# Optimization experiments

Hardware: AMD Instinct MI355X
Metric: run time of the kernel (lower is better)

The kernel has to match this reference:

```python
import jax, jax.numpy as jnp
import numpy as np
import math

B, N, D, H, FF, L = 256, 200, 128, 8, 512, 2
KD = D // H  # key/val dim per head
NEG_INF = -1e30  # used via -jnp.inf where safe


def setup_inputs() -> dict:
    key = jax.random.key(0)
    ks = jax.random.split(key, 32)
    s = 0.08
    inp = {
        "coords": jax.random.uniform(ks[0], (B, N, 2), jnp.float32),
        "demand": jax.random.uniform(ks[1], (B, N), jnp.float32) * 0.01,
        # init embeddings
        "w_depot": jax.random.normal(ks[2], (2, D), jnp.float32) * s,
        "b_depot": jax.random.normal(ks[3], (D,), jnp.float32) * s,
        "w_init": jax.random.normal(ks[4], (3, D), jnp.float32) * s,
        "b_init": jax.random.normal(ks[5], (D,), jnp.float32) * s,
        # encoder layers (stacked over L)
        "Wq": jax.random.normal(ks[6], (L, H, D, KD), jnp.float32) * s,
        "Wk": jax.random.normal(ks[7], (L, H, D, KD), jnp.float32) * s,
        "Wv": jax.random.normal(ks[8], (L, H, D, KD), jnp.float32) * s,
        "Wo": jax.random.normal(ks[9], (L, H, KD, D), jnp.float32) * s,
        "ff1_w": jax.random.normal(ks[10], (L, D, FF), jnp.float32) * s,
        "ff1_b": jax.random.normal(ks[11], (L, FF), jnp.float32) * s,
        "ff2_w": jax.random.normal(ks[12], (L, FF, D), jnp.float32) * s,
        "ff2_b": jax.random.normal(ks[13], (L, D), jnp.float32) * s,
        "n1_g": jnp.ones((L, D), jnp.float32),
        "n1_b": jnp.zeros((L, D), jnp.float32),
        "n2_g": jnp.ones((L, D), jnp.float32),
        "n2_b": jnp.zeros((L, D), jnp.float32),
        # decoder projections
        "w_proj_nodes": jax.random.normal(ks[14], (D, 3 * D), jnp.float32) * s,
        "w_fixed": jax.random.normal(ks[15], (D, D), jnp.float32) * s,
        "w_step": jax.random.normal(ks[16], (D + 1, D), jnp.float32) * s,
        "w_out": jax.random.normal(ks[17], (D, D), jnp.float32) * s,
    }
    return inp


def _batch_norm(x, g, b):
    # torch BatchNorm1d on flattened (B*N, D), training-mode batch stats
    m = x.mean(axis=(0, 1))
    v = x.var(axis=(0, 1))
    return g * (x - m) * jax.lax.rsqrt(v + 1e-5) + b


def _mha(x, Wq, Wk, Wv, Wo):
    # x: [B,N,D]; W*: [H,D,KD]; Wo: [H,KD,D]
    Q = jnp.einsum('bni,hik->hbnk', x, Wq)
    K = jnp.einsum('bni,hik->hbnk', x, Wk)
    V = jnp.einsum('bni,hik->hbnk', x, Wv)
    scale = 1.0 / math.sqrt(KD)
    attn = jax.nn.softmax(scale * jnp.einsum('hbnk,hbmk->hbnm', Q, K), axis=-1)
    heads = jnp.einsum('hbnm,hbmk->hbnk', attn, V)
    return jnp.einsum('hbnk,hkd->bnd', heads, Wo)


def _forward(coords, demand, w_depot, b_depot, w_init, b_init,
             Wq, Wk, Wv, Wo, ff1_w, ff1_b, ff2_w, ff2_b,
             n1_g, n1_b, n2_g, n2_b, w_proj_nodes, w_fixed, w_step, w_out):
    # ---- _init_embed ----
    depot_emb = coords[:, :1, :2] @ w_depot + b_depot                      # [B,1,D]
    node_feat = jnp.concatenate([coords[:, 1:, :], demand[:, 1:, None]], -1)
    node_emb = node_feat @ w_init + b_init                                 # [B,N-1,D]
    h = jnp.concatenate([depot_emb, node_emb], axis=1)                     # [B,N,D]

    # ---- GraphAttentionEncoder ----
    for l in range(L):
        h = _batch_norm(h + _mha(h, Wq[l], Wk[l], Wv[l], Wo[l]), n1_g[l], n1_b[l])
        ff = jnp.maximum(h @ ff1_w[l] + ff1_b[l], 0.0) @ ff2_w[l] + ff2_b[l]
        h = _batch_norm(h + ff, n2_g[l], n2_b[l])

    # ---- _precompute ----
    fixed_ctx = h.mean(axis=1) @ w_fixed                                   # [B,D]
    proj = h @ w_proj_nodes                                                # [B,N,3D]
    gk, gv, lk = jnp.split(proj, 3, axis=-1)
    gk = gk.reshape(B, N, H, KD).transpose(2, 0, 1, 3)                     # [H,B,N,KD]
    gv = gv.reshape(B, N, H, KD).transpose(2, 0, 1, 3)                     # [H,B,N,KD]

    inv_sqrt_kd = 1.0 / math.sqrt(KD)
    inv_sqrt_d = 1.0 / math.sqrt(D)
    barange = jnp.arange(B)

    def step(carry, _):
        visited, cur, used = carry
        cur_emb = h[barange, cur]                                          # [B,D]
        ctx = jnp.concatenate([cur_emb, (1.0 - used)[:, None]], -1)        # [B,D+1]
        q = fixed_ctx + ctx @ w_step                                       # [B,D]
        qh = q.reshape(B, H, KD).transpose(1, 0, 2)                        # [H,B,KD]
        compat = jnp.einsum('hbk,hbnk->hbn', qh, gk) * inv_sqrt_kd         # [H,B,N]
        compat = jnp.where(visited[None], -jnp.inf, compat)                # mask_inner
        attn = jax.nn.softmax(compat, axis=-1)
        gl = jnp.einsum('hbn,hbnk->hbk', attn, gv)                         # [H,B,KD]
        final_q = gl.transpose(1, 0, 2).reshape(B, D) @ w_out              # [B,D]
        logits = jnp.einsum('bd,bnd->bn', final_q, lk) * inv_sqrt_d
        logits = jnp.tanh(logits) * 10.0                                   # tanh_clipping
        logits = jnp.where(visited, -jnp.inf, logits)                      # mask_logits
        logp = jax.nn.log_softmax(logits, axis=-1)                         # temp = 1.0
        sel = jnp.argmax(logp, axis=-1)                                    # greedy decode
        visited = visited.at[barange, sel].set(True)
        used = used + demand[barange, sel]
        return (visited, sel, used), (logp, sel)

    visited0 = jnp.zeros((B, N), bool).at[:, 0].set(True)  # start at depot
    cur0 = jnp.zeros((B,), jnp.int32)
    used0 = jnp.zeros((B,), jnp.float32)
    _, (logps, sels) = jax.lax.scan(step, (visited0, cur0, used0), None, length=N - 1)
    log_p = logps.transpose(1, 0, 2)   # [B, N-1, N]
    pi = sels.transpose(1, 0)          # [B, N-1]
    return log_p, pi


def reference(coords, demand, w_depot, b_depot, w_init, b_init,
              Wq, Wk, Wv, Wo, ff1_w, ff1_b, ff2_w, ff2_b,
              n1_g, n1_b, n2_g, n2_b, w_proj_nodes, w_fixed, w_step, w_out):
    return _forward(coords, demand, w_depot, b_depot, w_init, b_init,
                    Wq, Wk, Wv, Wo, ff1_w, ff1_b, ff2_w, ff2_b,
                    n1_g, n1_b, n2_g, n2_b, w_proj_nodes, w_fixed, w_step, w_out)
```

## Files before the change

kernel.cpp:

```cpp
#include <hip/hip_runtime.h>
#include <math.h>

#define NB 256
#define NN 200
#define ND 128
#define NH 8
#define NFF 512
#define MROWS (NB*NN)

#define NEG_BIG (-1.0e30f)

#define GBM 128
#define GBN 128
#define GBK 16
__global__ __launch_bounds__(256) void k_gemm(const float* __restrict__ A,
    const float* __restrict__ B, const float* __restrict__ bias,
    float* __restrict__ C, int M, int N, int K, int flags)
{
  __shared__ float As[GBK][GBM];
  __shared__ float Bs[GBK][GBN];
  const int t = threadIdx.x;
  const int tx = t & 15, ty = t >> 4;
  const int row0 = blockIdx.y * GBM, col0 = blockIdx.x * GBN;
  float acc[8][8] = {};
  for (int k0 = 0; k0 < K; k0 += GBK) {
    {
      int m = t >> 1, kb = (t & 1) * 8;
      const float* src = A + (size_t)(row0 + m) * K + k0 + kb;
      float4 v0 = *(const float4*)(src);
      float4 v1 = *(const float4*)(src + 4);
      As[kb+0][m] = v0.x; As[kb+1][m] = v0.y; As[kb+2][m] = v0.z; As[kb+3][m] = v0.w;
      As[kb+4][m] = v1.x; As[kb+5][m] = v1.y; As[kb+6][m] = v1.z; As[kb+7][m] = v1.w;
    }
    {
      int kk = t >> 4, nb = (t & 15) * 8;
      const float* src = B + (size_t)(k0 + kk) * N + col0 + nb;
      float4 v0 = *(const float4*)(src);
      float4 v1 = *(const float4*)(src + 4);
      *(float4*)&Bs[kk][nb]   = v0;
      *(float4*)&Bs[kk][nb+4] = v1;
    }
    __syncthreads();
    #pragma unroll
    for (int kk = 0; kk < GBK; ++kk) {
      float a[8], bv[8];
      *(float4*)&a[0]  = *(const float4*)&As[kk][ty*8];
      *(float4*)&a[4]  = *(const float4*)&As[kk][ty*8+4];
      *(float4*)&bv[0] = *(const float4*)&Bs[kk][tx*8];
      *(float4*)&bv[4] = *(const float4*)&Bs[kk][tx*8+4];
      #pragma unroll
      for (int i = 0; i < 8; ++i)
        #pragma unroll
        for (int j = 0; j < 8; ++j)
          acc[i][j] += a[i] * bv[j];
    }
    __syncthreads();
  }
  #pragma unroll
  for (int i = 0; i < 8; ++i) {
    int r = row0 + ty*8 + i;
    float* crow = C + (size_t)r * N + col0 + tx*8;
    #pragma unroll
    for (int j = 0; j < 8; ++j) {
      float v = acc[i][j];
      if (bias) v += bias[col0 + tx*8 + j];
      if (flags & 1) v += crow[j];
      if (flags & 2) v = fmaxf(v, 0.0f);
      crow[j] = v;
    }
  }
}

__global__ void k_pack_wqkv(const float* __restrict__ Wq, const float* __restrict__ Wk,
                            const float* __restrict__ Wv, float* __restrict__ outp)
{
  int idx = blockIdx.x * 256 + threadIdx.x;
  if (idx >= 2*128*384) return;
  int l = idx / (128*384); int r = idx % (128*384);
  int d = r / 384; int j = r % 384;
  int sel = j >> 7; int hk = j & 127; int h = hk >> 4; int k = hk & 15;
  const float* W = sel == 0 ? Wq : (sel == 1 ? Wk : Wv);
  outp[idx] = W[((size_t)(l*8 + h)*128 + d)*16 + k];
}

__global__ void k_init(const float* __restrict__ coords, const float* __restrict__ demand,
                       const float* __restrict__ w_depot, const float* __restrict__ b_depot,
                       const float* __restrict__ w_init, const float* __restrict__ b_init,
                       float* __restrict__ h)
{
  int idx = blockIdx.x * 256 + threadIdx.x;
  if (idx >= NB*NN*ND) return;
  int d = idx & 127; int bn = idx >> 7; int n = bn % NN; int b = bn / NN;
  float cx = coords[(size_t)(b*NN + n)*2], cy = coords[(size_t)(b*NN + n)*2 + 1];
  float v;
  if (n == 0) v = cx*w_depot[d] + cy*w_depot[128+d] + b_depot[d];
  else        v = cx*w_init[d] + cy*w_init[128+d] + demand[b*NN+n]*w_init[256+d] + b_init[d];
  h[idx] = v;
}

__global__ __launch_bounds__(256) void k_attn(const float* __restrict__ qkv, float* __restrict__ out)
{
  __shared__ float Qs[NN][16], Ks[NN][16], Vs[NN][16];
  __shared__ float Ss[32][NN];
  const int b = blockIdx.x >> 3, hd = blockIdx.x & 7;
  const int t = threadIdx.x;
  const float* base = qkv + (size_t)b * NN * 384 + hd * 16;
  for (int e = t; e < NN * 16; e += 256) {
    int n = e >> 4, k = e & 15;
    const float* p = base + (size_t)n * 384;
    Qs[n][k] = p[k];
    Ks[n][k] = p[128 + k];
    Vs[n][k] = p[256 + k];
  }
  __syncthreads();
  const int i = t >> 3;
  const int jl = t & 7;
  for (int i0 = 0; i0 < NN; i0 += 32) {
    int ii = i0 + i;
    if (ii < NN) {
      float4 q0 = *(const float4*)&Qs[ii][0];
      float4 q1 = *(const float4*)&Qs[ii][4];
      float4 q2 = *(const float4*)&Qs[ii][8];
      float4 q3 = *(const float4*)&Qs[ii][12];
      for (int j = jl; j < NN; j += 8) {
        const float* kr = &Ks[j][0];
        float s = q0.x*kr[0] + q0.y*kr[1] + q0.z*kr[2]  + q0.w*kr[3]
                + q1.x*kr[4] + q1.y*kr[5] + q1.z*kr[6]  + q1.w*kr[7]
                + q2.x*kr[8] + q2.y*kr[9] + q2.z*kr[10] + q2.w*kr[11]
                + q3.x*kr[12]+ q3.y*kr[13]+ q3.z*kr[14] + q3.w*kr[15];
        Ss[i][j] = s * 0.25f;
      }
      float m = -INFINITY;
      for (int j = jl; j < NN; j += 8) m = fmaxf(m, Ss[i][j]);
      m = fmaxf(m, __shfl_xor(m, 1));
      m = fmaxf(m, __shfl_xor(m, 2));
      m = fmaxf(m, __shfl_xor(m, 4));
      float sum = 0.f;
      for (int j = jl; j < NN; j += 8) { float p = expf(Ss[i][j] - m); Ss[i][j] = p; sum += p; }
      sum += __shfl_xor(sum, 1);
      sum += __shfl_xor(sum, 2);
      sum += __shfl_xor(sum, 4);
      float inv = 1.0f / sum;
      float a0 = 0.f, a1 = 0.f;
      int k0 = jl * 2;
      for (int j = 0; j < NN; ++j) {
        float p = Ss[i][j];
        a0 += p * Vs[j][k0];
        a1 += p * Vs[j][k0+1];
      }
      float* o = out + ((size_t)b * NN + ii) * ND + hd * 16 + k0;
      o[0] = a0 * inv; o[1] = a1 * inv;
    }
  }
}

__global__ __launch_bounds__(256) void k_bn_stats(const float* __restrict__ x, float* __restrict__ partial)
{
  int jb = blockIdx.x, t = threadIdx.x;
  int c = t & 127, half = t >> 7;
  const float* base = x + (size_t)jb * NN * ND;
  float s = 0.f, ss = 0.f;
  for (int r = half; r < NN; r += 2) {
    float v = base[(size_t)r * ND + c];
    s += v; ss += v * v;
  }
  __shared__ float s1[256], s2[256];
  s1[t] = s; s2[t] = ss;
  __syncthreads();
  if (t < 128) {
    partial[(size_t)jb*128 + t]         = s1[t] + s1[t+128];
    partial[32768 + (size_t)jb*128 + t] = s2[t] + s2[t+128];
  }
}

__global__ void k_bn_finish(const float* __restrict__ partial, const float* __restrict__ g,
                            const float* __restrict__ bb, float* __restrict__ scsh)
{
  int c = threadIdx.x;
  float s = 0.f, ss = 0.f;
  for (int jb = 0; jb < 256; ++jb) {
    s  += partial[jb*128 + c];
    ss += partial[32768 + jb*128 + c];
  }
  float mean = s * (1.0f/51200.0f);
  float var  = ss * (1.0f/51200.0f) - mean*mean;
  float sc = g[c] * rsqrtf(var + 1e-5f);
  scsh[c] = sc;
  scsh[128 + c] = bb[c] - mean * sc;
}

__global__ void k_bn_apply(float* __restrict__ x, const float* __restrict__ scsh)
{
  int idx = blockIdx.x * 256 + threadIdx.x;
  if (idx >= NB*NN*ND) return;
  int c = idx & 127;
  x[idx] = x[idx] * scsh[c] + scsh[128 + c];
}

__global__ __launch_bounds__(256) void k_mean(const float* __restrict__ h, float* __restrict__ meanh)
{
  int b = blockIdx.x, t = threadIdx.x;
  int d = t & 127, half = t >> 7;
  float s = 0.f;
  for (int n = half; n < NN; n += 2) s += h[((size_t)b*NN + n)*ND + d];
  __shared__ float sm[256];
  sm[t] = s;
  __syncthreads();
  if (t < 128) meanh[b*ND + t] = (sm[t] + sm[t+128]) * (1.0f/200.0f);
}

__global__ __launch_bounds__(1024) void k_decode(
    const float* __restrict__ proj, const float* __restrict__ hproj,
    const float* __restrict__ fixedc, const float* __restrict__ w_step,
    const float* __restrict__ w_out, const float* __restrict__ demand,
    float* __restrict__ out_logp, float* __restrict__ out_pi)
{
  const int b = blockIdx.x;
  const int t = threadIdx.x;
  __shared__ __align__(16) float q[ND];
  __shared__ __align__(16) float fq[ND];
  __shared__ float fc[ND], wlast[ND];
  __shared__ float cmat[NH][NN];
  __shared__ float logits[NN];
  __shared__ float glp[8][ND], gl[ND];
  __shared__ float fqp[8][ND];
  __shared__ int idxl[NN];
  __shared__ int upos[NN];
  __shared__ int visited[NN];
  __shared__ int curs;
  __shared__ float useds;
  __shared__ float redf[16];
  __shared__ int redi[16];
  __shared__ float selv_s, lse_s;
  __shared__ int seln_s;

  if (t < ND) { fc[t] = fixedc[b*ND + t]; wlast[t] = w_step[128*ND + t]; }
  if (t < NN) {
    visited[t] = (t == 0) ? 1 : 0;
    upos[t] = t - 1;
    if (t < NN - 1) idxl[t] = t + 1;
  }
  if (t == 0) { curs = 0; useds = 0.0f; }
  __syncthreads();

  const float* pb = proj + (size_t)b * NN * 384;
  const int g = t >> 4, j16 = t & 15;
  const int qi = j16 * 4;

  int U = NN - 1;
  for (int step = 0; step < NN - 1; ++step) {
    if (t < ND) q[t] = fc[t] + hproj[((size_t)b*NN + curs)*ND + t] + (1.0f - useds)*wlast[t];
    __syncthreads();

    for (int u = g; u < U; u += 64) {
      const float* row = pb + (size_t)idxl[u]*384;
      float4 r0 = *(const float4*)(row + qi);
      float4 r1 = *(const float4*)(row + 64 + qi);
      float4 qa = *(const float4*)(q + qi);
      float4 qb = *(const float4*)(q + 64 + qi);
      float p0 = r0.x*qa.x + r0.y*qa.y + r0.z*qa.z + r0.w*qa.w;
      float p1 = r1.x*qb.x + r1.y*qb.y + r1.z*qb.z + r1.w*qb.w;
      p0 += __shfl_xor(p0, 1); p0 += __shfl_xor(p0, 2);
      p1 += __shfl_xor(p1, 1); p1 += __shfl_xor(p1, 2);
      if ((j16 & 3) == 0) {
        cmat[j16 >> 2][u]       = p0 * 0.25f;
        cmat[4 + (j16 >> 2)][u] = p1 * 0.25f;
      }
    }
    __syncthreads();

    if (t < 256) {
      int h = t >> 5, l5 = t & 31;
      float m = -INFINITY;
      for (int u = l5; u < U; u += 32) m = fmaxf(m, cmat[h][u]);
      #pragma unroll
      for (int mm = 1; mm < 32; mm <<= 1) m = fmaxf(m, __shfl_xor(m, mm));
      float s = 0.f;
      for (int u = l5; u < U; u += 32) { float p = expf(cmat[h][u] - m); cmat[h][u] = p; s += p; }
      #pragma unroll
      for (int mm = 1; mm < 32; mm <<= 1) s += __shfl_xor(s, mm);
      float inv = 1.0f / s;
      for (int u = l5; u < U; u += 32) cmat[h][u] *= inv;
    }
    __syncthreads();

    {
      int c = t >> 7, i = t & 127;
      float acc = 0.f;
      int hh = i >> 4;
      for (int u = c; u < U; u += 8) acc += cmat[hh][u] * pb[(size_t)idxl[u]*384 + 128 + i];
      glp[c][i] = acc;
    }
    __syncthreads();
    if (t < ND)
      gl[t] = ((glp[0][t] + glp[1][t]) + (glp[2][t] + glp[3][t]))
            + ((glp[4][t] + glp[5][t]) + (glp[6][t] + glp[7][t]));
    __syncthreads();

    {
      int c = t >> 7, d = t & 127;
      float acc = 0.f;
      const float* wb = w_out + (size_t)(c*16)*ND + d;
      #pragma unroll
      for (int i = 0; i < 16; ++i) acc += gl[c*16 + i] * wb[(size_t)i*ND];
      fqp[c][d] = acc;
    }
    __syncthreads();
    if (t < ND)
      fq[t] = ((fqp[0][t] + fqp[1][t]) + (fqp[2][t] + fqp[3][t]))
            + ((fqp[4][t] + fqp[5][t]) + (fqp[6][t] + fqp[7][t]));
    __syncthreads();

    for (int u = g; u < U; u += 64) {
      const float* row = pb + (size_t)idxl[u]*384 + 256;
      float4 r0 = *(const float4*)(row + qi);
      float4 r1 = *(const float4*)(row + 64 + qi);
      float4 fa = *(const float4*)(fq + qi);
      float4 fb = *(const float4*)(fq + 64 + qi);
      float p = r0.x*fa.x + r0.y*fa.y + r0.z*fa.z + r0.w*fa.w
              + r1.x*fb.x + r1.y*fb.y + r1.z*fb.z + r1.w*fb.w;
      p += __shfl_xor(p, 1); p += __shfl_xor(p, 2);
      p += __shfl_xor(p, 4); p += __shfl_xor(p, 8);
      if (j16 == 0) logits[u] = tanhf(p * 0.088388347648318447f) * 10.0f;
    }
    __syncthreads();

    float mv = -INFINITY; int mn = 0x7fffffff;
    for (int u = t; u < U; u += 1024) {
      float v = logits[u]; int n = idxl[u];
      if (v > mv || (v == mv && n < mn)) { mv = v; mn = n; }
    }
    #pragma unroll
    for (int mm = 1; mm < 64; mm <<= 1) {
      float ov = __shfl_xor(mv, mm); int on = __shfl_xor(mn, mm);
      if (ov > mv || (ov == mv && on < mn)) { mv = ov; mn = on; }
    }
    if ((t & 63) == 0) { redf[t >> 6] = mv; redi[t >> 6] = mn; }
    __syncthreads();
    if (t == 0) {
      for (int w = 1; w < 16; ++w)
        if (redf[w] > mv || (redf[w] == mv && redi[w] < mn)) { mv = redf[w]; mn = redi[w]; }
      selv_s = mv; seln_s = mn;
    }
    __syncthreads();
    float gmax = selv_s;
    float se = 0.f;
    for (int u = t; u < U; u += 1024) se += expf(logits[u] - gmax);
    #pragma unroll
    for (int mm = 1; mm < 64; mm <<= 1) se += __shfl_xor(se, mm);
    if ((t & 63) == 0) redf[t >> 6] = se;
    __syncthreads();
    if (t == 0) {
      float s = 0.f;
      for (int w = 0; w < 16; ++w) s += redf[w];
      lse_s = gmax + logf(s);
    }
    __syncthreads();
    float lse = lse_s;

    float* orow = out_logp + ((size_t)b*(NN-1) + step)*NN;
    if (t < NN) {
      int u = upos[t];
      float lv = logits[u < 0 ? 0 : u] - lse;
      orow[t] = visited[t] ? NEG_BIG : lv;
    }
    __syncthreads();
    if (t == 0) {
      int sel = seln_s;
      out_pi[(size_t)b*(NN-1) + step] = (float)sel;
      int us = upos[sel];
      int last = idxl[U-1];
      idxl[us] = last;
      upos[last] = us;
      visited[sel] = 1;
      upos[sel] = -1;
      curs = sel;
      useds += demand[b*NN + sel];
    }
    __syncthreads();
    --U;
  }
}

extern "C" void kernel_launch(void* const* d_in, const int* in_sizes, int n_in,
                              void* d_out, int out_size, void* d_ws, size_t ws_size,
                              hipStream_t stream)
{
  (void)in_sizes; (void)n_in; (void)out_size; (void)ws_size;
  const float* coords  = (const float*)d_in[0];
  const float* demand  = (const float*)d_in[1];
  const float* w_depot = (const float*)d_in[2];
  const float* b_depot = (const float*)d_in[3];
  const float* w_init  = (const float*)d_in[4];
  const float* b_init  = (const float*)d_in[5];
  const float* Wq      = (const float*)d_in[6];
  const float* Wk      = (const float*)d_in[7];
  const float* Wv      = (const float*)d_in[8];
  const float* Wo      = (const float*)d_in[9];
  const float* ff1w    = (const float*)d_in[10];
  const float* ff1b    = (const float*)d_in[11];
  const float* ff2w    = (const float*)d_in[12];
  const float* ff2b    = (const float*)d_in[13];
  const float* n1g     = (const float*)d_in[14];
  const float* n1b     = (const float*)d_in[15];
  const float* n2g     = (const float*)d_in[16];
  const float* n2b     = (const float*)d_in[17];
  const float* wproj   = (const float*)d_in[18];
  const float* wfixed  = (const float*)d_in[19];
  const float* wstep   = (const float*)d_in[20];
  const float* wout    = (const float*)d_in[21];
  float* out = (float*)d_out;

  float* ws = (float*)d_ws;
  float* h       = ws;
  float* big     = h + 6553600;
  float* attnout = big + (size_t)MROWS * 384;
  float* hproj   = attnout;
  float* meanh   = big + 26214400;
  float* fixedc  = meanh + 32768;
  float* bnpart  = fixedc + 32768;
  float* scsh    = bnpart + 65536;
  float* wqkvp   = scsh + 256;

  k_pack_wqkv<<<(2*128*384 + 255)/256, 256, 0, stream>>>(Wq, Wk, Wv, wqkvp);
  k_init<<<(NB*NN*ND + 255)/256, 256, 0, stream>>>(coords, demand, w_depot, b_depot, w_init, b_init, h);

  for (int l = 0; l < 2; ++l) {
    k_gemm<<<dim3(384/GBN, MROWS/GBM), 256, 0, stream>>>(h, wqkvp + l*49152, nullptr, big, MROWS, 384, 128, 0);
    k_attn<<<NB*NH, 256, 0, stream>>>(big, attnout);
    k_gemm<<<dim3(1, MROWS/GBM), 256, 0, stream>>>(attnout, Wo + l*16384, nullptr, h, MROWS, 128, 128, 1);
    k_bn_stats<<<256, 256, 0, stream>>>(h, bnpart);
    k_bn_finish<<<1, 128, 0, stream>>>(bnpart, n1g + l*128, n1b + l*128, scsh);
    k_bn_apply<<<(NB*NN*ND + 255)/256, 256, 0, stream>>>(h, scsh);
    k_gemm<<<dim3(512/GBN, MROWS/GBM), 256, 0, stream>>>(h, ff1w + l*65536, ff1b + l*512, big, MROWS, 512, 128, 2);
    k_gemm<<<dim3(1, MROWS/GBM), 256, 0, stream>>>(big, ff2w + l*65536, ff2b + l*128, h, MROWS, 128, 512, 1);
    k_bn_stats<<<256, 256, 0, stream>>>(h, bnpart);
    k_bn_finish<<<1, 128, 0, stream>>>(bnpart, n2g + l*128, n2b + l*128, scsh);
    k_bn_apply<<<(NB*NN*ND + 255)/256, 256, 0, stream>>>(h, scsh);
  }

  k_mean<<<NB, 256, 0, stream>>>(h, meanh);
  k_gemm<<<dim3(1, 256/GBM), 256, 0, stream>>>(meanh, wfixed, nullptr, fixedc, 256, 128, 128, 0);
  k_gemm<<<dim3(384/GBN, MROWS/GBM), 256, 0, stream>>>(h, wproj, nullptr, big, MROWS, 384, 128, 0);
  k_gemm<<<dim3(1, MROWS/GBM), 256, 0, stream>>>(h, wstep, nullptr, hproj, MROWS, 128, 128, 0);

  k_decode<<<NB, 1024, 0, stream>>>(big, hproj, fixedc, wstep, wout, demand,
                                    out, out + (size_t)NB*(NN-1)*NN);
}
```

Baseline: 4.131 ms.

## Cache per-batch decoder keys and values in registers across decode steps

```diff
diff --git a/kernel.cpp b/kernel.cpp
--- a/kernel.cpp
+++ b/kernel.cpp
@@ -209,7 +209,7 @@
   if (t < 128) meanh[b*ND + t] = (sm[t] + sm[t+128]) * (1.0f/200.0f);
 }
 
-__global__ __launch_bounds__(1024) void k_decode(
+__global__ __launch_bounds__(512, 2) void k_decode(
     const float* __restrict__ proj, const float* __restrict__ hproj,
     const float* __restrict__ fixedc, const float* __restrict__ w_step,
     const float* __restrict__ w_out, const float* __restrict__ demand,
@@ -219,52 +219,70 @@
   const int t = threadIdx.x;
   __shared__ __align__(16) float q[ND];
   __shared__ __align__(16) float fq[ND];
-  __shared__ float fc[ND], wlast[ND];
+  __shared__ float fc[ND], wlast[ND], dem[NN];
   __shared__ float cmat[NH][NN];
   __shared__ float logits[NN];
-  __shared__ float glp[8][ND], gl[ND];
-  __shared__ float fqp[8][ND];
-  __shared__ int idxl[NN];
-  __shared__ int upos[NN];
+  __shared__ float glp[4][ND], gl[ND];
+  __shared__ float fqp[4][ND];
   __shared__ int visited[NN];
   __shared__ int curs;
   __shared__ float useds;
-  __shared__ float redf[16];
-  __shared__ int redi[16];
+  __shared__ float redf[8];
+  __shared__ int redi[8];
   __shared__ float selv_s, lse_s;
   __shared__ int seln_s;
-
-  if (t < ND) { fc[t] = fixedc[b*ND + t]; wlast[t] = w_step[128*ND + t]; }
-  if (t < NN) {
-    visited[t] = (t == 0) ? 1 : 0;
-    upos[t] = t - 1;
-    if (t < NN - 1) idxl[t] = t + 1;
-  }
-  if (t == 0) { curs = 0; useds = 0.0f; }
-  __syncthreads();
 
   const float* pb = proj + (size_t)b * NN * 384;
   const int g = t >> 4, j16 = t & 15;
   const int qi = j16 * 4;
-
-  int U = NN - 1;
+  const int c = t >> 7, i = t & 127;
+
+  if (t < ND) { fc[t] = fixedc[b*ND + t]; wlast[t] = w_step[128*ND + t]; }
+  if (t < NN) { visited[t] = (t == 0) ? 1 : 0; dem[t] = demand[b*NN + t]; }
+  if (t == 0) { curs = 0; useds = 0.0f; }
+
+  float4 ka[7], kb_[7], la[7], lb[7];
+  #pragma unroll
+  for (int r = 0; r < 7; ++r) {
+    int n = g + 32*r;
+    if (n < NN) {
+      const float* row = pb + (size_t)n * 384;
+      ka[r]  = *(const float4*)(row + qi);
+      kb_[r] = *(const float4*)(row + 64 + qi);
+      la[r]  = *(const float4*)(row + 256 + qi);
+      lb[r]  = *(const float4*)(row + 256 + 64 + qi);
+    } else {
+      ka[r] = float4{0,0,0,0}; kb_[r] = float4{0,0,0,0};
+      la[r] = float4{0,0,0,0}; lb[r]  = float4{0,0,0,0};
+    }
+  }
+  float gvr[50];
+  #pragma unroll
+  for (int k = 0; k < 50; ++k)
+    gvr[k] = pb[(size_t)(c + 4*k)*384 + 128 + i];
+  __syncthreads();
+
   for (int step = 0; step < NN - 1; ++step) {
     if (t < ND) q[t] = fc[t] + hproj[((size_t)b*NN + curs)*ND + t] + (1.0f - useds)*wlast[t];
     __syncthreads();
 
-    for (int u = g; u < U; u += 64) {
-      const float* row = pb + (size_t)idxl[u]*384;
-      float4 r0 = *(const float4*)(row + qi);
-      float4 r1 = *(const float4*)(row + 64 + qi);
+    {
       float4 qa = *(const float4*)(q + qi);
       float4 qb = *(const float4*)(q + 64 + qi);
-      float p0 = r0.x*qa.x + r0.y*qa.y + r0.z*qa.z + r0.w*qa.w;
-      float p1 = r1.x*qb.x + r1.y*qb.y + r1.z*qb.z + r1.w*qb.w;
-      p0 += __shfl_xor(p0, 1); p0 += __shfl_xor(p0, 2);
-      p1 += __shfl_xor(p1, 1); p1 += __shfl_xor(p1, 2);
-      if ((j16 & 3) == 0) {
-        cmat[j16 >> 2][u]       = p0 * 0.25f;
-        cmat[4 + (j16 >> 2)][u] = p1 * 0.25f;
+      #pragma unroll
+      for (int r = 0; r < 7; ++r) {
+        int n = g + 32*r;
+        if (n < NN) {
+          float p0 = ka[r].x*qa.x + ka[r].y*qa.y + ka[r].z*qa.z + ka[r].w*qa.w;
+          float p1 = kb_[r].x*qb.x + kb_[r].y*qb.y + kb_[r].z*qb.z + kb_[r].w*qb.w;
+          p0 += __shfl_xor(p0, 1); p0 += __shfl_xor(p0, 2);
+          p1 += __shfl_xor(p1, 1); p1 += __shfl_xor(p1, 2);
+          if ((j16 & 3) == 0) {
+            bool vis = visited[n] != 0;
+            cmat[j16 >> 2][n]       = vis ? -1.0e30f : p0 * 0.25f;
+            cmat[4 + (j16 >> 2)][n] = vis ? -1.0e30f : p1 * 0.25f;
+          }
+        }
       }
     }
     __syncthreads();
@@ -272,113 +290,104 @@
     if (t < 256) {
       int h = t >> 5, l5 = t & 31;
       float m = -INFINITY;
-      for (int u = l5; u < U; u += 32) m = fmaxf(m, cmat[h][u]);
+      for (int n = l5; n < NN; n += 32) m = fmaxf(m, cmat[h][n]);
       #pragma unroll
       for (int mm = 1; mm < 32; mm <<= 1) m = fmaxf(m, __shfl_xor(m, mm));
       float s = 0.f;
-      for (int u = l5; u < U; u += 32) { float p = expf(cmat[h][u] - m); cmat[h][u] = p; s += p; }
+      for (int n = l5; n < NN; n += 32) { float p = expf(cmat[h][n] - m); cmat[h][n] = p; s += p; }
       #pragma unroll
       for (int mm = 1; mm < 32; mm <<= 1) s += __shfl_xor(s, mm);
       float inv = 1.0f / s;
-      for (int u = l5; u < U; u += 32) cmat[h][u] *= inv;
-    }
-    __syncthreads();
-
-    {
-      int c = t >> 7, i = t & 127;
+      for (int n = l5; n < NN; n += 32) cmat[h][n] *= inv;
+    }
+    __syncthreads();
+
+    {
+      int hh = i >> 4;
+      const float* pm = &cmat[hh][0];
       float acc = 0.f;
-      int hh = i >> 4;
-      for (int u = c; u < U; u += 8) acc += cmat[hh][u] * pb[(size_t)idxl[u]*384 + 128 + i];
+      #pragma unroll
+      for (int k = 0; k < 50; ++k)
+        acc += pm[c + 4*k] * gvr[k];
       glp[c][i] = acc;
     }
     __syncthreads();
-    if (t < ND)
-      gl[t] = ((glp[0][t] + glp[1][t]) + (glp[2][t] + glp[3][t]))
-            + ((glp[4][t] + glp[5][t]) + (glp[6][t] + glp[7][t]));
-    __syncthreads();
-
-    {
-      int c = t >> 7, d = t & 127;
+    if (t < ND) gl[t] = (glp[0][t] + glp[1][t]) + (glp[2][t] + glp[3][t]);
+    __syncthreads();
+
+    {
       float acc = 0.f;
-      const float* wb = w_out + (size_t)(c*16)*ND + d;
-      #pragma unroll
-      for (int i = 0; i < 16; ++i) acc += gl[c*16 + i] * wb[(size_t)i*ND];
-      fqp[c][d] = acc;
-    }
-    __syncthreads();
-    if (t < ND)
-      fq[t] = ((fqp[0][t] + fqp[1][t]) + (fqp[2][t] + fqp[3][t]))
-            + ((fqp[4][t] + fqp[5][t]) + (fqp[6][t] + fqp[7][t]));
-    __syncthreads();
-
-    for (int u = g; u < U; u += 64) {
-      const float* row = pb + (size_t)idxl[u]*384 + 256;
-      float4 r0 = *(const float4*)(row + qi);
-      float4 r1 = *(const float4*)(row + 64 + qi);
+      const float* wb = w_out + (size_t)(c*32)*ND + i;
+      #pragma unroll
+      for (int k = 0; k < 32; ++k) acc += gl[c*32 + k] * wb[(size_t)k*ND];
+      fqp[c][i] = acc;
+    }
+    __syncthreads();
+    if (t < ND) fq[t] = (fqp[0][t] + fqp[1][t]) + (fqp[2][t] + fqp[3][t]);
+    __syncthreads();
+
+    {
       float4 fa = *(const float4*)(fq + qi);
       float4 fb = *(const float4*)(fq + 64 + qi);
-      float p = r0.x*fa.x + r0.y*fa.y + r0.z*fa.z + r0.w*fa.w
-              + r1.x*fb.x + r1.y*fb.y + r1.z*fb.z + r1.w*fb.w;
-      p += __shfl_xor(p, 1); p += __shfl_xor(p, 2);
-      p += __shfl_xor(p, 4); p += __shfl_xor(p, 8);
-      if (j16 == 0) logits[u] = tanhf(p * 0.088388347648318447f) * 10.0f;
-    }
-    __syncthreads();
-
-    float mv = -INFINITY; int mn = 0x7fffffff;
-    for (int u = t; u < U; u += 1024) {
-      float v = logits[u]; int n = idxl[u];
-      if (v > mv || (v == mv && n < mn)) { mv = v; mn = n; }
-    }
-    #pragma unroll
-    for (int mm = 1; mm < 64; mm <<= 1) {
-      float ov = __shfl_xor(mv, mm); int on = __shfl_xor(mn, mm);
-      if (ov > mv || (ov == mv && on < mn)) { mv = ov; mn = on; }
-    }
-    if ((t & 63) == 0) { redf[t >> 6] = mv; redi[t >> 6] = mn; }
-    __syncthreads();
-    if (t == 0) {
-      for (int w = 1; w < 16; ++w)
-        if (redf[w] > mv || (redf[w] == mv && redi[w] < mn)) { mv = redf[w]; mn = redi[w]; }
-      selv_s = mv; seln_s = mn;
-    }
-    __syncthreads();
-    float gmax = selv_s;
-    float se = 0.f;
-    for (int u = t; u < U; u += 1024) se += expf(logits[u] - gmax);
-    #pragma unroll
-    for (int mm = 1; mm < 64; mm <<= 1) se += __shfl_xor(se, mm);
-    if ((t & 63) == 0) redf[t >> 6] = se;
-    __syncthreads();
-    if (t == 0) {
-      float s = 0.f;
-      for (int w = 0; w < 16; ++w) s += redf[w];
-      lse_s = gmax + logf(s);
-    }
-    __syncthreads();
+      #pragma unroll
+      for (int r = 0; r < 7; ++r) {
+        int n = g + 32*r;
+        if (n < NN) {
+          float p = la[r].x*fa.x + la[r].y*fa.y + la[r].z*fa.z + la[r].w*fa.w
+                  + lb[r].x*fb.x + lb[r].y*fb.y + lb[r].z*fb.z + lb[r].w*fb.w;
+          p += __shfl_xor(p, 1); p += __shfl_xor(p, 2);
+          p += __shfl_xor(p, 4); p += __shfl_xor(p, 8);
+          if (j16 == 0)
+            logits[n] = visited[n] ? -1.0e30f : tanhf(p * 0.088388347648318447f) * 10.0f;
+        }
+      }
+    }
+    __syncthreads();
+
+    {
+      float mv = (t < NN) ? logits[t] : -INFINITY;
+      int   mn = (t < NN) ? t : 0x7fffffff;
+      #pragma unroll
+      for (int mm = 1; mm < 64; mm <<= 1) {
+        float ov = __shfl_xor(mv, mm); int on = __shfl_xor(mn, mm);
+        if (ov > mv || (ov == mv && on < mn)) { mv = ov; mn = on; }
+      }
+      if ((t & 63) == 0) { redf[t >> 6] = mv; redi[t >> 6] = mn; }
+      __syncthreads();
+      if (t == 0) {
+        for (int w = 1; w < 8; ++w)
+          if (redf[w] > mv || (redf[w] == mv && redi[w] < mn)) { mv = redf[w]; mn = redi[w]; }
+        selv_s = mv; seln_s = mn;
+      }
+      __syncthreads();
+    }
+    {
+      float gmax = selv_s;
+      float se = (t < NN) ? expf(logits[t] - gmax) : 0.f;
+      #pragma unroll
+      for (int mm = 1; mm < 64; mm <<= 1) se += __shfl_xor(se, mm);
+      if ((t & 63) == 0) redf[t >> 6] = se;
+      __syncthreads();
+      if (t == 0) {
+        float s = 0.f;
+        for (int w = 0; w < 8; ++w) s += redf[w];
+        lse_s = gmax + logf(s);
+      }
+      __syncthreads();
+    }
     float lse = lse_s;
 
     float* orow = out_logp + ((size_t)b*(NN-1) + step)*NN;
-    if (t < NN) {
-      int u = upos[t];
-      float lv = logits[u < 0 ? 0 : u] - lse;
-      orow[t] = visited[t] ? NEG_BIG : lv;
-    }
+    if (t < NN) orow[t] = visited[t] ? NEG_BIG : logits[t] - lse;
     __syncthreads();
     if (t == 0) {
       int sel = seln_s;
       out_pi[(size_t)b*(NN-1) + step] = (float)sel;
-      int us = upos[sel];
-      int last = idxl[U-1];
-      idxl[us] = last;
-      upos[last] = us;
       visited[sel] = 1;
-      upos[sel] = -1;
       curs = sel;
-      useds += demand[b*NN + sel];
-    }
-    __syncthreads();
-    --U;
+      useds += dem[sel];
+    }
+    __syncthreads();
   }
 }
 
@@ -444,6 +453,6 @@
   k_gemm<<<dim3(384/GBN, MROWS/GBM), 256, 0, stream>>>(h, wproj, nullptr, big, MROWS, 384, 128, 0);
   k_gemm<<<dim3(1, MROWS/GBM), 256, 0, stream>>>(h, wstep, nullptr, hproj, MROWS, 128, 128, 0);
 
-  k_decode<<<NB, 1024, 0, stream>>>(big, hproj, fixedc, wstep, wout, demand,
-                                    out, out + (size_t)NB*(NN-1)*NN);
-}
+  k_decode<<<NB, 512, 0, stream>>>(big, hproj, fixedc, wstep, wout, demand,
+                                   out, out + (size_t)NB*(NN-1)*NN);
+}
```

After: 3.461 ms. -16.2%, faster.
